# Performance work log

Hardware: AMD Instinct MI355X
Metric: run time of the kernel (lower is better)

Reference implementation:

```python
import jax, jax.numpy as jnp
import numpy as np

N_NODES = 50000
N_EDGES = 800000
N_GRAPHS = 64
F0 = 64          # num_features
HID = 512        # hidden_size
N_OUT = 1


def setup_inputs() -> dict:
    key = jax.random.key(0)
    ks = jax.random.split(key, 16)

    def p(k, shape, scale):
        return jax.random.normal(k, shape, jnp.float32) * scale

    inp = {}
    inp["feature"] = jax.random.normal(ks[0], (N_NODES, F0), jnp.float32)
    inp["edge_index"] = jax.random.randint(ks[1], (2, N_EDGES), 0, N_NODES)
    inp["protein_batch"] = jnp.sort(jax.random.randint(ks[2], (N_NODES,), 0, N_GRAPHS))

    dims = [(F0, F0), (F0, 2 * F0), (2 * F0, 4 * F0)]
    for i, (din, dout) in enumerate(dims):
        s = 1.0 / np.sqrt(din)
        inp[f"W{i+1}"] = p(ks[3 + 3 * i], (din, dout), s)      # GATConv lin weight
        inp[f"att{i+1}"] = p(ks[4 + 3 * i], (2, dout), 0.1)    # [att_src; att_dst]
        inp[f"b{i+1}"] = jnp.zeros((dout,), jnp.float32)       # GATConv bias
    inp["fc1_w"] = p(ks[12], (4 * F0, HID), 1.0 / np.sqrt(4 * F0))
    inp["fc1_b"] = jnp.zeros((HID,), jnp.float32)
    inp["fc2_w"] = p(ks[13], (HID, N_OUT), 1.0 / np.sqrt(HID))
    inp["fc2_b"] = jnp.zeros((N_OUT,), jnp.float32)
    return inp


def _gat_conv(x, src, dst, W, att, b):
    """PyG GATConv, heads=1, concat=True, negative_slope=0.2 (self-loops already in src/dst)."""
    h = x @ W                                             # [N, Dout]
    # per-edge attention logit: a_src . h_j + a_dst . h_i
    alpha = jax.nn.leaky_relu(h @ att[0], 0.2 * 0 + 0.0)  # placeholder, replaced below
    logit = jax.nn.leaky_relu((h @ att[0])[src] + (h @ att[1])[dst], negative_slope=0.2)  # [E]
    # segment softmax over edges grouped by destination node
    m = jax.ops.segment_max(logit, dst, num_segments=N_NODES)      # [N]
    e = jnp.exp(logit - m[dst])                                    # [E]
    s = jax.ops.segment_sum(e, dst, num_segments=N_NODES)          # [N]
    coef = e / s[dst]                                              # [E]
    out = jax.ops.segment_sum(coef[:, None] * h[src], dst, num_segments=N_NODES)  # [N, Dout]
    return out + b


def reference(feature, edge_index, protein_batch,
              W1, att1, b1, W2, att2, b2, W3, att3, b3,
              fc1_w, fc1_b, fc2_w, fc2_b):
    loop = jnp.arange(N_NODES)
    src = jnp.concatenate([edge_index[0], loop])   # add_self_loops=True
    dst = jnp.concatenate([edge_index[1], loop])

    x = jax.nn.relu(_gat_conv(feature, src, dst, W1, att1, b1))
    x = jax.nn.relu(_gat_conv(x, src, dst, W2, att2, b2))
    x = jax.nn.relu(_gat_conv(x, src, dst, W3, att3, b3))

    # global mean pool per graph
    sums = jax.ops.segment_sum(x, protein_batch, num_segments=N_GRAPHS)          # [G, 4F]
    cnts = jax.ops.segment_sum(jnp.ones((N_NODES,), x.dtype), protein_batch,
                               num_segments=N_GRAPHS)                            # [G]
    gc = sums / jnp.maximum(cnts, 1.0)[:, None]

    gc = jax.nn.relu(gc @ fc1_w + fc1_b)   # dropout is identity at inference
    return gc @ fc2_w + fc2_b
```

## Files before the change

### kernel.cpp

```cpp
#include <hip/hip_runtime.h>
#include <hip/hip_bf16.h>

#define N_NODES 50000
#define N_EDGES 800000
#define E_TOT   850000
#define N_GRAPHS 64
#define HID 512

typedef unsigned short u16;
typedef __attribute__((ext_vector_type(8))) short short8;
typedef __attribute__((ext_vector_type(4))) float floatx4;
typedef union { uint4 u; short8 s; } frag_u;

__device__ inline unsigned f2b(float x) {
    unsigned u = __float_as_uint(x);
    return (u + 0x7fffu + ((u >> 16) & 1u)) >> 16;
}
__device__ inline float b2f_lo(unsigned u) { return __uint_as_float(u << 16); }
__device__ inline float b2f_hi(unsigned u) { return __uint_as_float(u & 0xffff0000u); }

__global__ __launch_bounds__(256) void count_kernel(const int* __restrict__ dst_e,
                                                    int* __restrict__ cnt,
                                                    int* __restrict__ order) {
    int e = blockIdx.x * 256 + threadIdx.x;
    if (e >= E_TOT) return;
    int d = (e < N_EDGES) ? dst_e[e] : (e - N_EDGES);
    order[e] = atomicAdd(&cnt[d], 1);
}

__global__ __launch_bounds__(256) void scan_local(const int* __restrict__ cnt,
                                                  int* __restrict__ out,
                                                  int* __restrict__ blocksum, int n) {
    __shared__ int buf[256];
    int tid = threadIdx.x;
    int i = blockIdx.x * 256 + tid;
    int v = (i < n) ? cnt[i] : 0;
    buf[tid] = v;
    __syncthreads();
    for (int off = 1; off < 256; off <<= 1) {
        int t = (tid >= off) ? buf[tid - off] : 0;
        __syncthreads();
        buf[tid] += t;
        __syncthreads();
    }
    if (i < n) out[i] = buf[tid] - v;
    if (tid == 255) blocksum[blockIdx.x] = buf[255];
}

__global__ __launch_bounds__(256) void scan_block(const int* __restrict__ blocksum,
                                                  int* __restrict__ blockoff, int nb,
                                                  int* __restrict__ total_ptr) {
    __shared__ int buf[256];
    int tid = threadIdx.x;
    int v = (tid < nb) ? blocksum[tid] : 0;
    buf[tid] = v;
    __syncthreads();
    for (int off = 1; off < 256; off <<= 1) {
        int t = (tid >= off) ? buf[tid - off] : 0;
        __syncthreads();
        buf[tid] += t;
        __syncthreads();
    }
    blockoff[tid] = buf[tid] - v;
    if (tid == 255) *total_ptr = buf[255];
}

__global__ __launch_bounds__(256) void scan_add(int* __restrict__ row_ptr,
                                                const int* __restrict__ blockoff, int n) {
    int i = blockIdx.x * 256 + threadIdx.x;
    if (i < n) row_ptr[i] += blockoff[blockIdx.x];
}

__global__ __launch_bounds__(256) void fill_kernel(const int* __restrict__ edge_index,
                                                   const int* __restrict__ row_ptr,
                                                   const int* __restrict__ order,
                                                   int* __restrict__ col_idx) {
    int e = blockIdx.x * 256 + threadIdx.x;
    if (e >= E_TOT) return;
    int s, d;
    if (e < N_EDGES) { s = edge_index[e]; d = edge_index[N_EDGES + e]; }
    else             { s = e - N_EDGES;   d = s; }
    col_idx[row_ptr[d] + order[e]] = s;
}

struct PrepDesc {
    const float* W[3];
    const float* att[3];
    float* wsd[3];
    u16* Wt[3];
};

__global__ __launch_bounds__(256) void prep_kernel(PrepDesc d) {
    const int DIN[3]  = {64, 64, 128};
    const int DOUT[3] = {64, 128, 256};
    int b = blockIdx.x;
    if (b < 128) {
        int wg = (b * 256 + (int)threadIdx.x) >> 6;
        int lane = threadIdx.x & 63;
        int l = (wg < 128) ? 0 : (wg < 256) ? 1 : 2;
        int base = (l == 0) ? 0 : (l == 1) ? 128 : 256;
        int k = wg - base;
        int Din = DIN[l], Dout = DOUT[l];
        int half = (k >= Din) ? 1 : 0;
        int row = half ? (k - Din) : k;
        float s = 0.f;
        for (int j = lane; j < Dout; j += 64)
            s += d.W[l][(size_t)row * Dout + j] * d.att[l][half * Dout + j];
#pragma unroll
        for (int off = 32; off > 0; off >>= 1) s += __shfl_xor(s, off);
        if (lane == 0) d.wsd[l][k] = s;
    } else {
        int t = (b - 128) * 256 + (int)threadIdx.x;
        int l; int off;
        if (t < 4096)       { l = 0; off = t; }
        else if (t < 12288) { l = 1; off = t - 4096; }
        else if (t < 45056) { l = 2; off = t - 12288; }
        else return;
        int Din = DIN[l], Dout = DOUT[l];
        int row = off / Dout, j = off & (Dout - 1);
        d.Wt[l][(size_t)j * Din + row] = (u16)f2b(d.W[l][off]);
    }
}

__global__ __launch_bounds__(256) void cvt_lsld_kernel(const float* __restrict__ feature,
                                                       const float* __restrict__ wsd,
                                                       u16* __restrict__ Fb,
                                                       float* __restrict__ lsld) {
    int wid = (blockIdx.x * 256 + threadIdx.x) >> 6;
    int lane = threadIdx.x & 63;
    if (wid >= N_NODES) return;
    float h = feature[(size_t)wid * 64 + lane];
    float a0 = h * wsd[lane];
    float a1 = h * wsd[64 + lane];
#pragma unroll
    for (int off = 32; off > 0; off >>= 1) {
        a0 += __shfl_xor(a0, off);
        a1 += __shfl_xor(a1, off);
    }
    if (lane == 0) { lsld[wid] = a0; lsld[N_NODES + wid] = a1; }
    Fb[(size_t)wid * 64 + lane] = (u16)f2b(h);
}

template <int NN, int KK>
__global__ __launch_bounds__(256) void sgemm_mfma_kernel(const u16* __restrict__ A,
                                                         const u16* __restrict__ Bt,
                                                         u16* __restrict__ C,
                                                         const float* __restrict__ bias,
                                                         const float* __restrict__ wsd_next,
                                                         float* __restrict__ lsld_next,
                                                         int M) {
    constexpr int KSTEPS = KK / 32;
    const int lane = threadIdx.x & 63;
    const int w = threadIdx.x >> 6;
    const int c = lane & 15;
    const int q = lane >> 4;
    const int bn = blockIdx.y * 64;
    const int r0 = blockIdx.x * 128 + w * 32;
    int ar0 = r0 + c;      if (ar0 > M - 1) ar0 = M - 1;
    int ar1 = r0 + 16 + c; if (ar1 > M - 1) ar1 = M - 1;
    const u16* __restrict__ Ap0 = A + (size_t)ar0 * KK + q * 8;
    const u16* __restrict__ Ap1 = A + (size_t)ar1 * KK + q * 8;
    floatx4 acc[2][4];
#pragma unroll
    for (int i = 0; i < 2; ++i)
#pragma unroll
        for (int b = 0; b < 4; ++b) acc[i][b] = (floatx4){0.f, 0.f, 0.f, 0.f};
#pragma unroll
    for (int ks = 0; ks < KSTEPS; ++ks) {
        const int k0 = ks * 32;
        frag_u a0, a1, bf[4];
        a0.u = *(const uint4*)(Ap0 + k0);
        a1.u = *(const uint4*)(Ap1 + k0);
#pragma unroll
        for (int b = 0; b < 4; ++b)
            bf[b].u = *(const uint4*)(Bt + (size_t)(bn + b * 16 + c) * KK + q * 8 + k0);
#pragma unroll
        for (int b = 0; b < 4; ++b) {
            acc[0][b] = __builtin_amdgcn_mfma_f32_16x16x32_bf16(a0.s, bf[b].s, acc[0][b], 0, 0, 0);
            acc[1][b] = __builtin_amdgcn_mfma_f32_16x16x32_bf16(a1.s, bf[b].s, acc[1][b], 0, 0, 0);
        }
    }
    const bool has_next = (wsd_next != nullptr);
    float ps[2][4] = {}, pd[2][4] = {};
#pragma unroll
    for (int b = 0; b < 4; ++b) {
        const int col = bn + b * 16 + c;
        const float bsv = bias[col];
        const float wsv = has_next ? wsd_next[col] : 0.f;
        const float wdv = has_next ? wsd_next[NN + col] : 0.f;
#pragma unroll
        for (int i = 0; i < 2; ++i) {
#pragma unroll
            for (int g = 0; g < 4; ++g) {
                int r = r0 + i * 16 + q * 4 + g;
                if (r < M) {
                    float v = fmaxf(acc[i][b][g] + bsv, 0.f);
                    C[(size_t)r * NN + col] = (u16)f2b(v);
                    ps[i][g] += v * wsv;
                    pd[i][g] += v * wdv;
                }
            }
        }
    }
    if (has_next) {
#pragma unroll
        for (int i = 0; i < 2; ++i)
#pragma unroll
            for (int g = 0; g < 4; ++g) {
#pragma unroll
                for (int mm = 1; mm < 16; mm <<= 1) {
                    ps[i][g] += __shfl_xor(ps[i][g], mm);
                    pd[i][g] += __shfl_xor(pd[i][g], mm);
                }
            }
        if (c == 0) {
#pragma unroll
            for (int i = 0; i < 2; ++i)
#pragma unroll
                for (int g = 0; g < 4; ++g) {
                    int r = r0 + i * 16 + q * 4 + g;
                    if (r < M) {
                        atomicAdd(&lsld_next[r], ps[i][g]);
                        atomicAdd(&lsld_next[M + r], pd[i][g]);
                    }
                }
        }
    }
}

template <int D>
__global__ __launch_bounds__(256) void gather_fused_kernel(const u16* __restrict__ X,
                                                           const float* __restrict__ lsld,
                                                           const int* __restrict__ row_ptr,
                                                           const int* __restrict__ col_idx,
                                                           u16* __restrict__ out) {
    constexpr int L = D / 8;
    constexpr int P = 64 / L;
    __shared__ float2 ec_all[4][64];
    int wid = (blockIdx.x * 256 + threadIdx.x) >> 6;
    int lane = threadIdx.x & 63;
    if (wid >= N_NODES) return;
    float2* __restrict__ ec = ec_all[threadIdx.x >> 6];
    const int start = row_ptr[wid];
    const int end = row_ptr[wid + 1];
    const int deg = end - start;
    const float ldi = lsld[N_NODES + wid];
    const float* __restrict__ ls = lsld;
    const int eslot = lane / L;
    const int fidx = lane % L;
    float a[8] = {0.f, 0.f, 0.f, 0.f, 0.f, 0.f, 0.f, 0.f};

    auto fma8 = [&](float cc, uint4 v) {
        a[0] += cc * b2f_lo(v.x); a[1] += cc * b2f_hi(v.x);
        a[2] += cc * b2f_lo(v.y); a[3] += cc * b2f_hi(v.y);
        a[4] += cc * b2f_lo(v.z); a[5] += cc * b2f_hi(v.z);
        a[6] += cc * b2f_lo(v.w); a[7] += cc * b2f_hi(v.w);
    };

    if (deg <= 64) {
        int srcl = 0;
        float l = -3.0e38f;
        if (lane < deg) {
            srcl = col_idx[start + lane];
            float t = ls[srcl] + ldi;
            l = (t > 0.f) ? t : 0.2f * t;
        }
        float m = l;
#pragma unroll
        for (int off = 32; off > 0; off >>= 1) m = fmaxf(m, __shfl_xor(m, off));
        float e = (lane < deg) ? __expf(l - m) : 0.f;
        float s = e;
#pragma unroll
        for (int off = 32; off > 0; off >>= 1) s += __shfl_xor(s, off);
        ec[lane] = make_float2(e / s, __int_as_float(srcl));

        const int nsteps = (deg + P - 1) / P;
        for (int g0 = 0; g0 < nsteps; g0 += 4) {
            float2 p[4]; uint4 v[4];
#pragma unroll
            for (int j = 0; j < 4; ++j) {
                int idx = (g0 + j) * P + eslot;
                bool valid = idx < deg;
                p[j] = ec[valid ? idx : 0];
                if (!valid) p[j].x = 0.f;
            }
#pragma unroll
            for (int j = 0; j < 4; ++j)
                v[j] = *(const uint4*)(X + (size_t)__float_as_int(p[j].y) * D + fidx * 8);
#pragma unroll
            for (int j = 0; j < 4; ++j) fma8(p[j].x, v[j]);
        }
    } else {
        float m = -3.0e38f;
        for (int e = start + lane; e < end; e += 64) {
            float t = ls[col_idx[e]] + ldi;
            t = (t > 0.f) ? t : 0.2f * t;
            m = fmaxf(m, t);
        }
#pragma unroll
        for (int off = 32; off > 0; off >>= 1) m = fmaxf(m, __shfl_xor(m, off));
        float ssum = 0.f;
        for (int e = start + lane; e < end; e += 64) {
            float t = ls[col_idx[e]] + ldi;
            t = (t > 0.f) ? t : 0.2f * t;
            ssum += __expf(t - m);
        }
#pragma unroll
        for (int off = 32; off > 0; off >>= 1) ssum += __shfl_xor(ssum, off);
        const float inv = 1.0f / ssum;
        for (int e0 = start; e0 < end; e0 += P) {
            int e = e0 + eslot;
            if (e < end) {
                int src = col_idx[e];
                float t = ls[src] + ldi;
                t = (t > 0.f) ? t : 0.2f * t;
                float cc = __expf(t - m) * inv;
                uint4 v = *(const uint4*)(X + (size_t)src * D + fidx * 8);
                fma8(cc, v);
            }
        }
    }
#pragma unroll
    for (int mm = L; mm < 64; mm <<= 1) {
#pragma unroll
        for (int i = 0; i < 8; ++i) a[i] += __shfl_xor(a[i], mm);
    }
    if (lane < L) {
        uint4 o;
        o.x = f2b(a[0]) | (f2b(a[1]) << 16);
        o.y = f2b(a[2]) | (f2b(a[3]) << 16);
        o.z = f2b(a[4]) | (f2b(a[5]) << 16);
        o.w = f2b(a[6]) | (f2b(a[7]) << 16);
        *(uint4*)(out + (size_t)wid * D + lane * 8) = o;
    }
}

__device__ inline int lower_bound_dev(const int* __restrict__ a, int n, int v) {
    int lo = 0, hi = n;
    while (lo < hi) { int mid = (lo + hi) >> 1; if (a[mid] < v) lo = mid + 1; else hi = mid; }
    return lo;
}

#define POOL_SPLITS 32
__global__ __launch_bounds__(256) void pool_kernel(const u16* __restrict__ x3,
                                                   const int* __restrict__ batch,
                                                   float* __restrict__ gsum,
                                                   int* __restrict__ gcnt) {
    int g = blockIdx.x;
    int split = blockIdx.y;
    int tid = threadIdx.x;
    int start = lower_bound_dev(batch, N_NODES, g);
    int end = lower_bound_dev(batch, N_NODES, g + 1);
    int nodes = end - start;
    int n0 = start + (int)((long long)nodes * split / POOL_SPLITS);
    int n1 = start + (int)((long long)nodes * (split + 1) / POOL_SPLITS);
    float acc = 0.f;
    for (int n = n0; n < n1; ++n) acc += b2f_lo((unsigned)x3[(size_t)n * 256 + tid]);
    atomicAdd(&gsum[g * 256 + tid], acc);
    if (split == 0 && tid == 0) gcnt[g] = nodes;
}

__global__ __launch_bounds__(256) void fc1_kernel(const float* __restrict__ gsum,
                                                  const int* __restrict__ gcnt,
                                                  const float* __restrict__ w,
                                                  const float* __restrict__ b,
                                                  float* __restrict__ h1) {
    __shared__ float gc[256];
    int g = blockIdx.x;
    int tid = threadIdx.x;
    float denom = fmaxf((float)gcnt[g], 1.0f);
    gc[tid] = gsum[g * 256 + tid] / denom;
    __syncthreads();
#pragma unroll
    for (int jj = 0; jj < 2; ++jj) {
        int j = tid + jj * 256;
        float sum = b[j];
        for (int k = 0; k < 256; ++k) sum += gc[k] * w[k * HID + j];
        h1[g * HID + j] = (sum > 0.f) ? sum : 0.f;
    }
}

__global__ __launch_bounds__(256) void fc2_kernel(const float* __restrict__ h1,
                                                  const float* __restrict__ w,
                                                  const float* __restrict__ b,
                                                  float* __restrict__ out) {
    __shared__ float red[256];
    int g = blockIdx.x;
    int tid = threadIdx.x;
    float acc = h1[g * HID + tid] * w[tid] + h1[g * HID + tid + 256] * w[tid + 256];
    red[tid] = acc;
    __syncthreads();
    for (int off = 128; off > 0; off >>= 1) {
        if (tid < off) red[tid] += red[tid + off];
        __syncthreads();
    }
    if (tid == 0) out[g] = red[0] + b[0];
}

extern "C" void kernel_launch(void* const* d_in, const int* in_sizes, int n_in,
                              void* d_out, int out_size, void* d_ws, size_t ws_size,
                              hipStream_t stream) {
    const float* feature  = (const float*)d_in[0];
    const int*   edge_idx = (const int*)d_in[1];
    const int*   batch    = (const int*)d_in[2];
    const float* W1    = (const float*)d_in[3];
    const float* att1  = (const float*)d_in[4];
    const float* b1    = (const float*)d_in[5];
    const float* W2    = (const float*)d_in[6];
    const float* att2  = (const float*)d_in[7];
    const float* b2    = (const float*)d_in[8];
    const float* W3    = (const float*)d_in[9];
    const float* att3  = (const float*)d_in[10];
    const float* b3    = (const float*)d_in[11];
    const float* fc1_w = (const float*)d_in[12];
    const float* fc1_b = (const float*)d_in[13];
    const float* fc2_w = (const float*)d_in[14];
    const float* fc2_b = (const float*)d_in[15];
    float* out = (float*)d_out;

    char* w = (char*)d_ws;
    auto alloc = [&](size_t bytes) {
        char* p = w;
        w += (bytes + 255) & ~(size_t)255;
        return p;
    };
    u16* Fb    = (u16*)alloc((size_t)N_NODES * 64 * 2);
    u16* X1b   = (u16*)alloc((size_t)N_NODES * 64 * 2);
    u16* X2b   = (u16*)alloc((size_t)N_NODES * 128 * 2);
    u16* X3b   = (u16*)alloc((size_t)N_NODES * 256 * 2);
    u16* AGGb  = (u16*)alloc((size_t)N_NODES * 128 * 2);
    float* lsld1 = (float*)alloc((size_t)N_NODES * 2 * 4);
    char* zbase = w;
    int* cnt      = (int*)alloc((size_t)N_NODES * 4);
    float* gsum   = (float*)alloc(64 * 256 * 4);
    float* lsld23 = (float*)alloc((size_t)N_NODES * 4 * 4);
    size_t zbytes = (size_t)(w - zbase);
    float* lsld2 = lsld23;
    float* lsld3 = lsld23 + (size_t)N_NODES * 2;
    float* wsd1  = (float*)alloc(2 * 64 * 4);
    float* wsd2  = (float*)alloc(2 * 64 * 4);
    float* wsd3  = (float*)alloc(2 * 128 * 4);
    u16* Wt1   = (u16*)alloc(64 * 64 * 2);
    u16* Wt2   = (u16*)alloc(128 * 64 * 2);
    u16* Wt3   = (u16*)alloc(256 * 128 * 2);
    float* h1    = (float*)alloc(64 * HID * 4);
    int* row_ptr  = (int*)alloc((size_t)(N_NODES + 1) * 4);
    int* col_idx  = (int*)alloc((size_t)E_TOT * 4);
    int* order    = (int*)alloc((size_t)E_TOT * 4);
    int* blocksum = (int*)alloc(256 * 4);
    int* blockoff = (int*)alloc(256 * 4);
    int* gcnt     = (int*)alloc(64 * 4);

    hipMemsetAsync(zbase, 0, zbytes, stream);

    const int EB = (E_TOT + 255) / 256;
    const int NB = (N_NODES + 255) / 256;
    const int WB = (N_NODES * 64 + 255) / 256;
    const int GB = (N_NODES + 127) / 128;

    PrepDesc pd;
    pd.W[0] = W1; pd.W[1] = W2; pd.W[2] = W3;
    pd.att[0] = att1; pd.att[1] = att2; pd.att[2] = att3;
    pd.wsd[0] = wsd1; pd.wsd[1] = wsd2; pd.wsd[2] = wsd3;
    pd.Wt[0] = Wt1; pd.Wt[1] = Wt2; pd.Wt[2] = Wt3;
    prep_kernel<<<304, 256, 0, stream>>>(pd);

    count_kernel<<<EB, 256, 0, stream>>>(edge_idx + N_EDGES, cnt, order);
    scan_local<<<NB, 256, 0, stream>>>(cnt, row_ptr, blocksum, N_NODES);
    scan_block<<<1, 256, 0, stream>>>(blocksum, blockoff, NB, row_ptr + N_NODES);
    scan_add<<<NB, 256, 0, stream>>>(row_ptr, blockoff, N_NODES);
    fill_kernel<<<EB, 256, 0, stream>>>(edge_idx, row_ptr, order, col_idx);

    cvt_lsld_kernel<<<WB, 256, 0, stream>>>(feature, wsd1, Fb, lsld1);
    gather_fused_kernel<64><<<WB, 256, 0, stream>>>(Fb, lsld1, row_ptr, col_idx, AGGb);
    sgemm_mfma_kernel<64, 64><<<dim3(GB, 1), 256, 0, stream>>>(AGGb, Wt1, X1b, b1, wsd2, lsld2, N_NODES);

    gather_fused_kernel<64><<<WB, 256, 0, stream>>>(X1b, lsld2, row_ptr, col_idx, AGGb);
    sgemm_mfma_kernel<128, 64><<<dim3(GB, 2), 256, 0, stream>>>(AGGb, Wt2, X2b, b2, wsd3, lsld3, N_NODES);

    gather_fused_kernel<128><<<WB, 256, 0, stream>>>(X2b, lsld3, row_ptr, col_idx, AGGb);
    sgemm_mfma_kernel<256, 128><<<dim3(GB, 4), 256, 0, stream>>>(AGGb, Wt3, X3b, b3, nullptr, nullptr, N_NODES);

    pool_kernel<<<dim3(N_GRAPHS, POOL_SPLITS), 256, 0, stream>>>(X3b, batch, gsum, gcnt);
    fc1_kernel<<<N_GRAPHS, 256, 0, stream>>>(gsum, gcnt, fc1_w, fc1_b, h1);
    fc2_kernel<<<N_GRAPHS, 256, 0, stream>>>(h1, fc2_w, fc2_b, out);
}
```

Before: 336.3 us.

## Fuse CSR build and feature convert into persistent grid-barrier kernel; merge FC layers

Replaces the count, three-stage scan, fill and cvt_lsld kernels with one persistent 1024-block kernel. Its phases are separated by atomic-counter grid barriers, which removes several launches and their inter-kernel gaps. fc1 and fc2 are merged into one kernel that keeps the hidden vector in shared memory. The layer-3 GEMM uses 8 column tiles per block instead of 4, halving the grid's y dimension. The grid barrier assumes all 1024 blocks are co-resident, so it can deadlock if occupancy drops below that, and the spin waits add some synchronisation cost.

After: 671.6 us. +99.7%, slower.

```diff
diff --git a/kernel.cpp b/kernel.cpp
--- a/kernel.cpp
+++ b/kernel.cpp
@@ -6,6 +6,8 @@
 #define E_TOT   850000
 #define N_GRAPHS 64
 #define HID 512
+#define NBC 196
+#define CSRB 1024
 
 typedef unsigned short u16;
 typedef __attribute__((ext_vector_type(8))) short short8;
@@ -19,68 +21,99 @@
 __device__ inline float b2f_lo(unsigned u) { return __uint_as_float(u << 16); }
 __device__ inline float b2f_hi(unsigned u) { return __uint_as_float(u & 0xffff0000u); }
 
-__global__ __launch_bounds__(256) void count_kernel(const int* __restrict__ dst_e,
-                                                    int* __restrict__ cnt,
-                                                    int* __restrict__ order) {
-    int e = blockIdx.x * 256 + threadIdx.x;
-    if (e >= E_TOT) return;
-    int d = (e < N_EDGES) ? dst_e[e] : (e - N_EDGES);
-    order[e] = atomicAdd(&cnt[d], 1);
-}
-
-__global__ __launch_bounds__(256) void scan_local(const int* __restrict__ cnt,
-                                                  int* __restrict__ out,
-                                                  int* __restrict__ blocksum, int n) {
+__device__ inline void gbar(int* bar, int idx, int nb) {
+    __syncthreads();
+    if (threadIdx.x == 0) {
+        __threadfence();
+        __hip_atomic_fetch_add(&bar[idx], 1, __ATOMIC_ACQ_REL, __HIP_MEMORY_SCOPE_AGENT);
+        while (__hip_atomic_load(&bar[idx], __ATOMIC_ACQUIRE, __HIP_MEMORY_SCOPE_AGENT) < nb)
+            __builtin_amdgcn_s_sleep(2);
+        __threadfence();
+    }
+    __syncthreads();
+}
+
+__global__ __launch_bounds__(256, 4) void csr_cvt_kernel(const int* __restrict__ edge_index,
+                                                         const float* __restrict__ feature,
+                                                         const float* __restrict__ wsd1,
+                                                         int* __restrict__ cnt,
+                                                         int* __restrict__ order,
+                                                         int* __restrict__ row_ptr,
+                                                         int* __restrict__ col_idx,
+                                                         u16* __restrict__ Fb,
+                                                         float* __restrict__ lsld1,
+                                                         int* __restrict__ blocksum,
+                                                         int* __restrict__ blockoff,
+                                                         int* __restrict__ bar) {
     __shared__ int buf[256];
-    int tid = threadIdx.x;
-    int i = blockIdx.x * 256 + tid;
-    int v = (i < n) ? cnt[i] : 0;
-    buf[tid] = v;
-    __syncthreads();
-    for (int off = 1; off < 256; off <<= 1) {
-        int t = (tid >= off) ? buf[tid - off] : 0;
+    const int tid = threadIdx.x;
+    const int gtid = blockIdx.x * 256 + tid;
+
+    for (int e = gtid; e < E_TOT; e += CSRB * 256) {
+        int d = (e < N_EDGES) ? edge_index[N_EDGES + e] : (e - N_EDGES);
+        order[e] = atomicAdd(&cnt[d], 1);
+    }
+    {
+        const int lane = tid & 63;
+        const int gw = gtid >> 6;
+        for (int wid = gw; wid < N_NODES; wid += (CSRB * 256) >> 6) {
+            float h = feature[(size_t)wid * 64 + lane];
+            float a0 = h * wsd1[lane];
+            float a1 = h * wsd1[64 + lane];
+#pragma unroll
+            for (int off = 32; off > 0; off >>= 1) {
+                a0 += __shfl_xor(a0, off);
+                a1 += __shfl_xor(a1, off);
+            }
+            if (lane == 0) { lsld1[wid] = a0; lsld1[N_NODES + wid] = a1; }
+            Fb[(size_t)wid * 64 + lane] = (u16)f2b(h);
+        }
+    }
+    gbar(bar, 0, CSRB);
+
+    if (blockIdx.x < NBC) {
+        int i = blockIdx.x * 256 + tid;
+        int v = (i < N_NODES) ? cnt[i] : 0;
+        buf[tid] = v;
         __syncthreads();
-        buf[tid] += t;
+        for (int off = 1; off < 256; off <<= 1) {
+            int t = (tid >= off) ? buf[tid - off] : 0;
+            __syncthreads();
+            buf[tid] += t;
+            __syncthreads();
+        }
+        if (i < N_NODES) row_ptr[i] = buf[tid] - v;
+        if (tid == 255) blocksum[blockIdx.x] = buf[255];
+    }
+    gbar(bar, 1, CSRB);
+
+    if (blockIdx.x == 0) {
+        int v = (tid < NBC) ? blocksum[tid] : 0;
+        buf[tid] = v;
         __syncthreads();
-    }
-    if (i < n) out[i] = buf[tid] - v;
-    if (tid == 255) blocksum[blockIdx.x] = buf[255];
-}
-
-__global__ __launch_bounds__(256) void scan_block(const int* __restrict__ blocksum,
-                                                  int* __restrict__ blockoff, int nb,
-                                                  int* __restrict__ total_ptr) {
-    __shared__ int buf[256];
-    int tid = threadIdx.x;
-    int v = (tid < nb) ? blocksum[tid] : 0;
-    buf[tid] = v;
-    __syncthreads();
-    for (int off = 1; off < 256; off <<= 1) {
-        int t = (tid >= off) ? buf[tid - off] : 0;
-        __syncthreads();
-        buf[tid] += t;
-        __syncthreads();
-    }
-    blockoff[tid] = buf[tid] - v;
-    if (tid == 255) *total_ptr = buf[255];
-}
-
-__global__ __launch_bounds__(256) void scan_add(int* __restrict__ row_ptr,
-                                                const int* __restrict__ blockoff, int n) {
-    int i = blockIdx.x * 256 + threadIdx.x;
-    if (i < n) row_ptr[i] += blockoff[blockIdx.x];
-}
-
-__global__ __launch_bounds__(256) void fill_kernel(const int* __restrict__ edge_index,
-                                                   const int* __restrict__ row_ptr,
-                                                   const int* __restrict__ order,
-                                                   int* __restrict__ col_idx) {
-    int e = blockIdx.x * 256 + threadIdx.x;
-    if (e >= E_TOT) return;
-    int s, d;
-    if (e < N_EDGES) { s = edge_index[e]; d = edge_index[N_EDGES + e]; }
-    else             { s = e - N_EDGES;   d = s; }
-    col_idx[row_ptr[d] + order[e]] = s;
+        for (int off = 1; off < 256; off <<= 1) {
+            int t = (tid >= off) ? buf[tid - off] : 0;
+            __syncthreads();
+            buf[tid] += t;
+            __syncthreads();
+        }
+        blockoff[tid] = buf[tid] - v;
+    }
+    gbar(bar, 2, CSRB);
+
+    if (blockIdx.x < NBC) {
+        int i = blockIdx.x * 256 + tid;
+        if (i < N_NODES) row_ptr[i] += blockoff[blockIdx.x];
+    }
+    if (gtid == 0) row_ptr[N_NODES] = E_TOT;
+    gbar(bar, 3, CSRB);
+
+    for (int e = gtid; e < E_TOT; e += CSRB * 256) {
+        int s, d;
+        if (e < N_EDGES) { s = edge_index[e]; d = edge_index[N_EDGES + e]; }
+        else             { s = e - N_EDGES;   d = s; }
+        col_idx[row_ptr[d] + order[e]] = s;
+    }
 }
 
 struct PrepDesc {
@@ -122,26 +155,7 @@
     }
 }
 
-__global__ __launch_bounds__(256) void cvt_lsld_kernel(const float* __restrict__ feature,
-                                                       const float* __restrict__ wsd,
-                                                       u16* __restrict__ Fb,
-                                                       float* __restrict__ lsld) {
-    int wid = (blockIdx.x * 256 + threadIdx.x) >> 6;
-    int lane = threadIdx.x & 63;
-    if (wid >= N_NODES) return;
-    float h = feature[(size_t)wid * 64 + lane];
-    float a0 = h * wsd[lane];
-    float a1 = h * wsd[64 + lane];
-#pragma unroll
-    for (int off = 32; off > 0; off >>= 1) {
-        a0 += __shfl_xor(a0, off);
-        a1 += __shfl_xor(a1, off);
-    }
-    if (lane == 0) { lsld[wid] = a0; lsld[N_NODES + wid] = a1; }
-    Fb[(size_t)wid * 64 + lane] = (u16)f2b(h);
-}
-
-template <int NN, int KK>
+template <int NN, int KK, int NT>
 __global__ __launch_bounds__(256) void sgemm_mfma_kernel(const u16* __restrict__ A,
                                                          const u16* __restrict__ Bt,
                                                          u16* __restrict__ C,
@@ -154,28 +168,28 @@
     const int w = threadIdx.x >> 6;
     const int c = lane & 15;
     const int q = lane >> 4;
-    const int bn = blockIdx.y * 64;
+    const int bn = blockIdx.y * (NT * 16);
     const int r0 = blockIdx.x * 128 + w * 32;
     int ar0 = r0 + c;      if (ar0 > M - 1) ar0 = M - 1;
     int ar1 = r0 + 16 + c; if (ar1 > M - 1) ar1 = M - 1;
     const u16* __restrict__ Ap0 = A + (size_t)ar0 * KK + q * 8;
     const u16* __restrict__ Ap1 = A + (size_t)ar1 * KK + q * 8;
-    floatx4 acc[2][4];
+    floatx4 acc[2][NT];
 #pragma unroll
     for (int i = 0; i < 2; ++i)
 #pragma unroll
-        for (int b = 0; b < 4; ++b) acc[i][b] = (floatx4){0.f, 0.f, 0.f, 0.f};
+        for (int b = 0; b < NT; ++b) acc[i][b] = (floatx4){0.f, 0.f, 0.f, 0.f};
 #pragma unroll
     for (int ks = 0; ks < KSTEPS; ++ks) {
         const int k0 = ks * 32;
-        frag_u a0, a1, bf[4];
+        frag_u a0, a1, bf[NT];
         a0.u = *(const uint4*)(Ap0 + k0);
         a1.u = *(const uint4*)(Ap1 + k0);
 #pragma unroll
-        for (int b = 0; b < 4; ++b)
+        for (int b = 0; b < NT; ++b)
             bf[b].u = *(const uint4*)(Bt + (size_t)(bn + b * 16 + c) * KK + q * 8 + k0);
 #pragma unroll
-        for (int b = 0; b < 4; ++b) {
+        for (int b = 0; b < NT; ++b) {
             acc[0][b] = __builtin_amdgcn_mfma_f32_16x16x32_bf16(a0.s, bf[b].s, acc[0][b], 0, 0, 0);
             acc[1][b] = __builtin_amdgcn_mfma_f32_16x16x32_bf16(a1.s, bf[b].s, acc[1][b], 0, 0, 0);
         }
@@ -183,7 +197,7 @@
     const bool has_next = (wsd_next != nullptr);
     float ps[2][4] = {}, pd[2][4] = {};
 #pragma unroll
-    for (int b = 0; b < 4; ++b) {
+    for (int b = 0; b < NT; ++b) {
         const int col = bn + b * 16 + c;
         const float bsv = bias[col];
         const float wsv = has_next ? wsd_next[col] : 0.f;
@@ -360,12 +374,16 @@
     if (split == 0 && tid == 0) gcnt[g] = nodes;
 }
 
-__global__ __launch_bounds__(256) void fc1_kernel(const float* __restrict__ gsum,
-                                                  const int* __restrict__ gcnt,
-                                                  const float* __restrict__ w,
-                                                  const float* __restrict__ b,
-                                                  float* __restrict__ h1) {
+__global__ __launch_bounds__(256) void fc_kernel(const float* __restrict__ gsum,
+                                                 const int* __restrict__ gcnt,
+                                                 const float* __restrict__ w1,
+                                                 const float* __restrict__ b1,
+                                                 const float* __restrict__ w2,
+                                                 const float* __restrict__ b2,
+                                                 float* __restrict__ out) {
     __shared__ float gc[256];
+    __shared__ float h1s[HID];
+    __shared__ float red[256];
     int g = blockIdx.x;
     int tid = threadIdx.x;
     float denom = fmaxf((float)gcnt[g], 1.0f);
@@ -374,27 +392,19 @@
 #pragma unroll
     for (int jj = 0; jj < 2; ++jj) {
         int j = tid + jj * 256;
-        float sum = b[j];
-        for (int k = 0; k < 256; ++k) sum += gc[k] * w[k * HID + j];
-        h1[g * HID + j] = (sum > 0.f) ? sum : 0.f;
-    }
-}
-
-__global__ __launch_bounds__(256) void fc2_kernel(const float* __restrict__ h1,
-                                                  const float* __restrict__ w,
-                                                  const float* __restrict__ b,
-                                                  float* __restrict__ out) {
-    __shared__ float red[256];
-    int g = blockIdx.x;
-    int tid = threadIdx.x;
-    float acc = h1[g * HID + tid] * w[tid] + h1[g * HID + tid + 256] * w[tid + 256];
+        float sum = b1[j];
+        for (int k = 0; k < 256; ++k) sum += gc[k] * w1[k * HID + j];
+        h1s[j] = (sum > 0.f) ? sum : 0.f;
+    }
+    __syncthreads();
+    float acc = h1s[tid] * w2[tid] + h1s[tid + 256] * w2[tid + 256];
     red[tid] = acc;
     __syncthreads();
     for (int off = 128; off > 0; off >>= 1) {
         if (tid < off) red[tid] += red[tid + off];
         __syncthreads();
     }
-    if (tid == 0) out[g] = red[0] + b[0];
+    if (tid == 0) out[g] = red[0] + b2[0];
 }
 
 extern "C" void kernel_launch(void* const* d_in, const int* in_sizes, int n_in,
@@ -434,6 +444,7 @@
     int* cnt      = (int*)alloc((size_t)N_NODES * 4);
     float* gsum   = (float*)alloc(64 * 256 * 4);
     float* lsld23 = (float*)alloc((size_t)N_NODES * 4 * 4);
+    int* bar      = (int*)alloc(16 * 4);
     size_t zbytes = (size_t)(w - zbase);
     float* lsld2 = lsld23;
     float* lsld3 = lsld23 + (size_t)N_NODES * 2;
@@ -443,7 +454,6 @@
     u16* Wt1   = (u16*)alloc(64 * 64 * 2);
     u16* Wt2   = (u16*)alloc(128 * 64 * 2);
     u16* Wt3   = (u16*)alloc(256 * 128 * 2);
-    float* h1    = (float*)alloc(64 * HID * 4);
     int* row_ptr  = (int*)alloc((size_t)(N_NODES + 1) * 4);
     int* col_idx  = (int*)alloc((size_t)E_TOT * 4);
     int* order    = (int*)alloc((size_t)E_TOT * 4);
@@ -453,8 +463,6 @@
 
     hipMemsetAsync(zbase, 0, zbytes, stream);
 
-    const int EB = (E_TOT + 255) / 256;
-    const int NB = (N_NODES + 255) / 256;
     const int WB = (N_NODES * 64 + 255) / 256;
     const int GB = (N_NODES + 127) / 128;
 
@@ -465,23 +473,19 @@
     pd.Wt[0] = Wt1; pd.Wt[1] = Wt2; pd.Wt[2] = Wt3;
     prep_kernel<<<304, 256, 0, stream>>>(pd);
 
-    count_kernel<<<EB, 256, 0, stream>>>(edge_idx + N_EDGES, cnt, order);
-    scan_local<<<NB, 256, 0, stream>>>(cnt, row_ptr, blocksum, N_NODES);
-    scan_block<<<1, 256, 0, stream>>>(blocksum, blockoff, NB, row_ptr + N_NODES);
-    scan_add<<<NB, 256, 0, stream>>>(row_ptr, blockoff, N_NODES);
-    fill_kernel<<<EB, 256, 0, stream>>>(edge_idx, row_ptr, order, col_idx);
-
-    cvt_lsld_kernel<<<WB, 256, 0, stream>>>(feature, wsd1, Fb, lsld1);
+    csr_cvt_kernel<<<CSRB, 256, 0, stream>>>(edge_idx, feature, wsd1,
+                                             cnt, order, row_ptr, col_idx,
+                                             Fb, lsld1, blocksum, blockoff, bar);
+
     gather_fused_kernel<64><<<WB, 256, 0, stream>>>(Fb, lsld1, row_ptr, col_idx, AGGb);
-    sgemm_mfma_kernel<64, 64><<<dim3(GB, 1), 256, 0, stream>>>(AGGb, Wt1, X1b, b1, wsd2, lsld2, N_NODES);
+    sgemm_mfma_kernel<64, 64, 4><<<dim3(GB, 1), 256, 0, stream>>>(AGGb, Wt1, X1b, b1, wsd2, lsld2, N_NODES);
 
     gather_fused_kernel<64><<<WB, 256, 0, stream>>>(X1b, lsld2, row_ptr, col_idx, AGGb);
-    sgemm_mfma_kernel<128, 64><<<dim3(GB, 2), 256, 0, stream>>>(AGGb, Wt2, X2b, b2, wsd3, lsld3, N_NODES);
+    sgemm_mfma_kernel<128, 64, 4><<<dim3(GB, 2), 256, 0, stream>>>(AGGb, Wt2, X2b, b2, wsd3, lsld3, N_NODES);
 
     gather_fused_kernel<128><<<WB, 256, 0, stream>>>(X2b, lsld3, row_ptr, col_idx, AGGb);
-    sgemm_mfma_kernel<256, 128><<<dim3(GB, 4), 256, 0, stream>>>(AGGb, Wt3, X3b, b3, nullptr, nullptr, N_NODES);
+    sgemm_mfma_kernel<256, 128, 8><<<dim3(GB, 2), 256, 0, stream>>>(AGGb, Wt3, X3b, b3, nullptr, nullptr, N_NODES);
 
     pool_kernel<<<dim3(N_GRAPHS, POOL_SPLITS), 256, 0, stream>>>(X3b, batch, gsum, gcnt);
-    fc1_kernel<<<N_GRAPHS, 256, 0, stream>>>(gsum, gcnt, fc1_w, fc1_b, h1);
-    fc2_kernel<<<N_GRAPHS, 256, 0, stream>>>(h1, fc2_w, fc2_b, out);
-}
+    fc_kernel<<<N_GRAPHS, 256, 0, stream>>>(gsum, gcnt, fc1_w, fc1_b, fc2_w, fc2_b, out);
+}
```
